# Optimization experiments

Measured on AMD Instinct MI355X. Metric: run time of the kernel, lower is better.

Reference implementation:

```python
import jax, jax.numpy as jnp
import numpy as np

B, N = 4, 500
C_DIM = 256            # content_dim == feat_channels
G = 4                  # n_groups
P_IN, P_OUT = 32, 128
EFF = C_DIM // G       # 64 = eff_in_dim = eff_out_dim
TOTAL = EFF * EFF + P_IN * P_OUT   # 8192 params per group per query
STRIDES = (8, 16, 32, 64)
LVL_SHAPES = ((100, 160), (50, 80), (25, 40), (13, 20))
TAU = 2.0
LVL_MAP = 3.0          # log2(STRIDES[0]): z -> fpn level index
EPS = 1e-5


def setup_inputs() -> dict:
    key = jax.random.key(0)
    ks = jax.random.split(key, 16)
    feats = [jax.random.normal(ks[i], (B, C_DIM, h, w), jnp.float32)
             for i, (h, w) in enumerate(LVL_SHAPES)]
    query_feat = jax.random.normal(ks[4], (B, N, C_DIM), jnp.float32)
    xy = jax.random.uniform(ks[5], (B, N, 2), jnp.float32, 50.0, 1000.0)
    z = jax.random.uniform(ks[6], (B, N, 1), jnp.float32, 3.0, 6.0)
    r = jax.random.uniform(ks[7], (B, N, 1), jnp.float32, -1.0, 1.0)
    query_xyzr = jnp.concatenate([xy, z, r], -1)
    w_off = jax.random.normal(ks[8], (C_DIM, P_IN * G * 3), jnp.float32) * 0.01
    b_off = jax.random.normal(ks[9], (P_IN * G * 3,), jnp.float32) * 0.1
    w_pg = jax.random.normal(ks[10], (C_DIM, G * TOTAL), jnp.float32) * 0.02
    b_pg = jax.random.normal(ks[11], (G * TOTAL,), jnp.float32) * 0.02
    w_out = jax.random.normal(ks[12], (G * P_OUT * EFF, C_DIM), jnp.float32) * 0.005
    b_out = jnp.zeros((C_DIM,), jnp.float32)
    ln_g = jnp.ones((C_DIM,), jnp.float32)
    ln_b = jnp.zeros((C_DIM,), jnp.float32)
    return dict(feat0=feats[0], feat1=feats[1], feat2=feats[2], feat3=feats[3],
                query_feat=query_feat, query_xyzr=query_xyzr,
                w_off=w_off, b_off=b_off, w_pg=w_pg, b_pg=b_pg,
                w_out=w_out, b_out=b_out, ln_g=ln_g, ln_b=ln_b)


def _ln2d(x):
    # F.layer_norm over last TWO dims, no affine
    mu = x.mean((-2, -1), keepdims=True)
    var = jnp.mean((x - mu) ** 2, (-2, -1), keepdims=True)
    return (x - mu) * jax.lax.rsqrt(var + EPS)


def _bilinear(feat, px, py):
    # torch grid_sample(bilinear, zeros padding, align_corners=False)
    # feat: [BG, H, W, Cg]; px, py: [BG, Q] pixel coords
    BGn, H, W, Cg = feat.shape
    fflat = feat.reshape(BGn, H * W, Cg)
    bidx = jnp.arange(BGn)[:, None]
    x0 = jnp.floor(px)
    y0 = jnp.floor(py)
    wx, wy = px - x0, py - y0
    x0i, y0i = x0.astype(jnp.int32), y0.astype(jnp.int32)

    def corner(xi, yi, w):
        valid = (xi >= 0) & (xi < W) & (yi >= 0) & (yi < H)
        idx = jnp.clip(yi, 0, H - 1) * W + jnp.clip(xi, 0, W - 1)
        return fflat[bidx, idx] * (w * valid)[..., None]

    return (corner(x0i, y0i, (1 - wx) * (1 - wy)) + corner(x0i + 1, y0i, wx * (1 - wy))
            + corner(x0i, y0i + 1, (1 - wx) * wy) + corner(x0i + 1, y0i + 1, wx * wy))


def _forward(feat0, feat1, feat2, feat3, query_feat, query_xyzr,
             w_off, b_off, w_pg, b_pg, w_out, b_out, ln_g, ln_b):
    feats = (feat0, feat1, feat2, feat3)
    # --- make_sample_points ---
    off = (query_feat @ w_off + b_off).reshape(B, N, G * P_IN, 3)
    cc = query_xyzr[..., :2]
    z = query_xyzr[..., 2:3]
    r = query_xyzr[..., 3:4]
    roi_wh = (2.0 ** z) * jnp.concatenate([2.0 ** (-0.5 * r), 2.0 ** (0.5 * r)], -1)  # [B,N,2]
    sample_xy = cc[:, :, None, :] + off[..., :2] * roi_wh[:, :, None, :]   # [B,N,G*P,2]
    sample_lvl = z[:, :, None, 0:1] + off[..., 2:3]                        # [B,N,G*P,1]

    # --- sampling_3d: softmax level weights ---
    lvl = sample_lvl[..., 0] - LVL_MAP                                     # [B,N,G*P]
    grid = jnp.arange(len(STRIDES), dtype=lvl.dtype)
    lw = jax.nn.softmax(-((lvl[..., None] - grid) ** 2) / TAU, axis=-1)    # [B,N,G*P,L]

    # regroup to per-group layout [B*G, N*P, ...]
    sx = sample_xy.reshape(B, N, G, P_IN, 2).transpose(0, 2, 1, 3, 4).reshape(B * G, N * P_IN, 2)
    lw_g = lw.reshape(B, N, G, P_IN, -1).transpose(0, 2, 1, 3, 4).reshape(B * G, N * P_IN, -1)

    sampled = jnp.zeros((B * G, N * P_IN, EFF), jnp.float32)
    for li, (feat, stride) in enumerate(zip(feats, STRIDES)):
        H, W = feat.shape[2], feat.shape[3]
        fg = feat.reshape(B * G, EFF, H, W).transpose(0, 2, 3, 1)  # [BG,H,W,EFF]
        nx = sx[..., 0] / (W * stride) * 2.0 - 1.0
        ny = sx[..., 1] / (H * stride) * 2.0 - 1.0
        px = (nx + 1.0) * 0.5 * W - 0.5
        py = (ny + 1.0) * 0.5 * H - 0.5
        sampled = sampled + _bilinear(fg, px, py) * lw_g[..., li][..., None]
    # [B,N,G,P,EFF]
    x = sampled.reshape(B, G, N, P_IN, EFF).transpose(0, 2, 1, 3, 4)

    # --- AdaptiveMixing ---
    params = (query_feat @ w_pg + b_pg).reshape(B * N, G, TOTAL)
    M = params[..., :EFF * EFF].reshape(B * N, G, EFF, EFF)
    S = params[..., EFF * EFF:].reshape(B * N, G, P_OUT, P_IN)
    out = x.reshape(B * N, G, P_IN, EFF)
    out = jax.nn.relu(_ln2d(jnp.einsum('bgpc,bgcd->bgpd', out, M)))  # channel mix
    out = jax.nn.relu(_ln2d(jnp.einsum('bgop,bgpd->bgod', S, out)))  # spatial mix
    out = out.reshape(B, N, G * P_OUT * EFF) @ w_out + b_out
    q = query_feat + out

    # --- final LayerNorm(content_dim) with affine ---
    mu = q.mean(-1, keepdims=True)
    var = jnp.mean((q - mu) ** 2, -1, keepdims=True)
    return (q - mu) * jax.lax.rsqrt(var + EPS) * ln_g + ln_b


def reference(feat0, feat1, feat2, feat3, query_feat, query_xyzr,
              w_off, b_off, w_pg, b_pg, w_out, b_out, ln_g, ln_b):
    return _forward(feat0, feat1, feat2, feat3, query_feat, query_xyzr,
                    w_off, b_off, w_pg, b_pg, w_out, b_out, ln_g, ln_b)
```

## Files before the change

### kernel.cpp

```cpp
#include <hip/hip_runtime.h>
#include <hip/hip_bf16.h>
#include <cstdint>
#include <cstddef>

#define DI __device__ __forceinline__

#define NN 500
#define NQ 2000
#define GTOT 32768
#define LN_EPS 1e-5f

typedef __attribute__((ext_vector_type(8))) short short8v;
typedef __attribute__((ext_vector_type(4))) float f32x4;
typedef const __attribute__((address_space(1))) void* gp1_t;
typedef __attribute__((address_space(3))) void* lp3_t;

DI unsigned short f2bf(float f){
  unsigned u = __float_as_uint(f);
  return (unsigned short)((u + 0x7fffu + ((u>>16)&1u)) >> 16);
}
DI float bf2f(unsigned short s){ return __uint_as_float(((unsigned)s)<<16); }

DI void bred256(float& s, float& s2, float* red, int tid){
  #pragma unroll
  for(int off=32; off; off>>=1){
    s  += __shfl_xor(s,  off, 64);
    s2 += __shfl_xor(s2, off, 64);
  }
  int w = tid>>6;
  if((tid&63)==0){ red[w*2]=s; red[w*2+1]=s2; }
  __syncthreads();
  s  = red[0]+red[2]+red[4]+red[6];
  s2 = red[1]+red[3]+red[5]+red[7];
  __syncthreads();
}

__global__ __launch_bounds__(256) void k_transpose(const float* __restrict__ src,
    unsigned short* __restrict__ dst, int H, int W){
  __shared__ float tile[64][161];
  int bg = blockIdx.x / H, h = blockIdx.x % H;
  int b = bg >> 2, g = bg & 3;
  const float* s = src + (((size_t)(b*256 + g*64))*H + h)*(size_t)W;
  for(int idx=threadIdx.x; idx<64*W; idx+=256){
    int c = idx / W, w = idx - c*W;
    tile[c][w] = s[(size_t)c*H*W + w];
  }
  __syncthreads();
  unsigned short* d = dst + ((size_t)bg*H + h)*(size_t)W*64;
  for(int idx=threadIdx.x; idx<64*W; idx+=256){
    int w = idx>>6, c = idx&63;
    d[idx] = f2bf(tile[c][w]);
  }
}

__global__ __launch_bounds__(384) void k_off(const float* __restrict__ qf,
    const float* __restrict__ xyzr, const float* __restrict__ w_off,
    const float* __restrict__ b_off, float2* __restrict__ xyb, float4* __restrict__ lwb){
  __shared__ float qs[8][256];
  __shared__ float os[8][384];
  int q0 = blockIdx.x*8, tid = threadIdx.x;
  for(int idx=tid; idx<2048; idx+=384){
    int qq = idx>>8, k = idx&255;
    qs[qq][k] = qf[(size_t)(q0+qq)*256 + k];
  }
  __syncthreads();
  {
    int j = tid;
    float acc[8];
    #pragma unroll
    for(int i=0;i<8;i++) acc[i]=0.f;
    for(int k=0;k<256;k++){
      float w = w_off[(size_t)k*384 + j];
      #pragma unroll
      for(int qq=0;qq<8;qq++) acc[qq] += qs[qq][k]*w;
    }
    float bb = b_off[j];
    #pragma unroll
    for(int qq=0;qq<8;qq++) os[qq][j] = acc[qq] + bb;
  }
  __syncthreads();
  for(int idx=tid; idx<1024; idx+=384){
    int qq = idx>>7, gp = idx&127;
    int q = q0+qq;
    float4 xr = *(const float4*)&xyzr[(size_t)q*4];
    float rw = exp2f(xr.z - 0.5f*xr.w);
    float rh = exp2f(xr.z + 0.5f*xr.w);
    float sx = xr.x + os[qq][gp*3+0]*rw;
    float sy = xr.y + os[qq][gp*3+1]*rh;
    float lvl = xr.z + os[qq][gp*3+2] - 3.0f;
    float d0=lvl, d1=lvl-1.f, d2=lvl-2.f, d3=lvl-3.f;
    float e0=-0.5f*d0*d0, e1=-0.5f*d1*d1, e2=-0.5f*d2*d2, e3=-0.5f*d3*d3;
    float m = fmaxf(fmaxf(e0,e1),fmaxf(e2,e3));
    float x0=expf(e0-m), x1=expf(e1-m), x2=expf(e2-m), x3=expf(e3-m);
    float inv = 1.f/(x0+x1+x2+x3);
    xyb[(size_t)q*128+gp] = make_float2(sx,sy);
    lwb[(size_t)q*128+gp] = make_float4(x0*inv, x1*inv, x2*inv, x3*inv);
  }
}

__global__ __launch_bounds__(256) void k_cvtqf(const float* __restrict__ qf,
    unsigned short* __restrict__ qfb){
  int idx = blockIdx.x*256 + threadIdx.x;
  size_t base = (size_t)idx*8;
  int row = idx >> 5;
  ushort4 lo, hi;
  if(row < NQ){
    float4 a = *(const float4*)(qf + base);
    float4 b = *(const float4*)(qf + base + 4);
    lo.x=f2bf(a.x); lo.y=f2bf(a.y); lo.z=f2bf(a.z); lo.w=f2bf(a.w);
    hi.x=f2bf(b.x); hi.y=f2bf(b.y); hi.z=f2bf(b.z); hi.w=f2bf(b.w);
  } else {
    lo.x=lo.y=lo.z=lo.w=0; hi.x=hi.y=hi.z=hi.w=0;
  }
  *(ushort4*)(qfb + base) = lo;
  *(ushort4*)(qfb + base + 4) = hi;
}

__global__ __launch_bounds__(256) void k_trcvt(const float* __restrict__ src,
    unsigned short* __restrict__ dst, int R, int C){
  __shared__ float tile[64][65];
  int ctiles = C >> 6;
  int rt = blockIdx.x / ctiles, ct = blockIdx.x % ctiles;
  int r0 = rt<<6, c0 = ct<<6;
  int tid = threadIdx.x;
  int lr = tid>>6, lc = tid&63;
  #pragma unroll
  for(int i=0;i<16;i++)
    tile[lr + i*4][lc] = src[(size_t)(r0+lr+i*4)*C + c0+lc];
  __syncthreads();
  #pragma unroll
  for(int i=0;i<16;i++)
    dst[(size_t)(c0+lr+i*4)*R + r0+lc] = f2bf(tile[lc][lr+i*4]);
}

DI f32x4 mfma16(short8v a, short8v b, f32x4 c){
  return __builtin_amdgcn_mfma_f32_16x16x32_bf16(a, b, c, 0, 0, 0);
}

DI int swz32(int c, int r){ return c ^ (r&3) ^ ((r>>2)&3); }

DI void stageG32(const unsigned short* __restrict__ g, size_t row0, size_t ldk,
                 size_t k0, unsigned short* lds, int tid){
  int wv = tid>>6;
  #pragma unroll
  for(int i=0;i<2;i++){
    int e = i*256 + tid;
    int r = e>>2, c = e&3;
    int cs = swz32(c, r);
    const unsigned short* gp = g + (row0 + (size_t)r)*ldk + k0 + (size_t)cs*8;
    unsigned short* lp = lds + (size_t)(i*256 + wv*64)*8;
    __builtin_amdgcn_global_load_lds((gp1_t)(const void*)gp, (lp3_t)(void*)lp, 16, 0, 0);
  }
}

DI short8v frag32(const unsigned short* lds, int row, int q4){
  return *(const short8v*)(lds + (size_t)row*32 + (size_t)swz32(q4, row)*8);
}

DI void mma32(const unsigned short* lsA, const unsigned short* lsB,
              int wm, int wn, int lane, f32x4 acc[4][4]){
  int r15 = lane&15, q4 = lane>>4;
  short8v a[4], b[4];
  #pragma unroll
  for(int i=0;i<4;i++){
    a[i] = frag32(lsA, wm*64 + i*16 + r15, q4);
    b[i] = frag32(lsB, wn*64 + i*16 + r15, q4);
  }
  #pragma unroll
  for(int mi=0;mi<4;mi++)
    #pragma unroll
    for(int ni=0;ni<4;ni++)
      acc[mi][ni] = mfma16(a[mi], b[ni], acc[mi][ni]);
}

DI int xcd_remap(int bid, int nwg){
  return ((bid & 7) * (nwg >> 3)) + (bid >> 3);
}

__global__ __launch_bounds__(256, 4) void k_pgemm_mfma(const unsigned short* __restrict__ qfb,
    const unsigned short* __restrict__ wpgT, const float* __restrict__ b_pg,
    unsigned short* __restrict__ par, int qbase, int qlim, int mtiles){
  __shared__ unsigned short pool[16384];
  int bid = xcd_remap(blockIdx.x, gridDim.x);
  int mt = bid % mtiles, nt = bid / mtiles;
  size_t m0 = (size_t)mt*128, n0 = (size_t)nt*128;
  int tid = threadIdx.x, lane = tid&63, wv = tid>>6;
  int wm = wv>>1, wn = wv&1;
  int r15 = lane&15, q4 = lane>>4;
  f32x4 acc[4][4] = {};
  stageG32(qfb,  qbase+m0, 256, 0, pool, tid);
  stageG32(wpgT, n0,       256, 0, pool + 8192, tid);
  __syncthreads();
  #pragma unroll
  for(int t=0; t<8; t++){
    int co = (t&1)*4096;
    if(t<7){
      int no = ((t&1)^1)*4096;
      stageG32(qfb,  qbase+m0, 256, (size_t)(t+1)*32, pool + no, tid);
      stageG32(wpgT, n0,       256, (size_t)(t+1)*32, pool + 8192 + no, tid);
    }
    mma32(pool + co, pool + 8192 + co, wm, wn, lane, acc);
    __syncthreads();
  }
  unsigned short* es = pool;
  #pragma unroll
  for(int h=0; h<2; ++h){
    if(h) __syncthreads();
    if(wn == h){
      #pragma unroll
      for(int ni=0; ni<4; ni++){
        float bias = b_pg[(int)n0 + wn*64 + ni*16 + r15];
        #pragma unroll
        for(int mi=0; mi<4; mi++)
          #pragma unroll
          for(int j=0; j<4; j++){
            int row = wm*64 + mi*16 + q4*4 + j;
            es[row*72 + ni*16 + r15] = f2bf(acc[mi][ni][j] + bias);
          }
      }
    }
    __syncthreads();
    #pragma unroll
    for(int i=0;i<4;i++){
      int e = i*256 + tid;
      int row = e>>3, c8 = (e&7)*8;
      int rl = (int)m0 + row;
      if(qbase + rl < qlim){
        uint4 v = *(const uint4*)(es + row*72 + c8);
        *(uint4*)&par[(size_t)rl*GTOT + n0 + h*64 + c8] = v;
      }
    }
  }
}

__global__ __launch_bounds__(256, 4) void k_fgemm_mfma(const unsigned short* __restrict__ Ag,
    const unsigned short* __restrict__ woutT, float* __restrict__ part,
    int qbase, int qlim, int mtiles, int kspl){
  __shared__ unsigned short pool[16384];
  int bid = xcd_remap(blockIdx.x, gridDim.x);
  int nt = bid & 1;
  int r2 = bid >> 1;
  int mt = r2 % mtiles, ks = r2 / mtiles;
  size_t m0 = (size_t)mt*128, n0 = (size_t)nt*128;
  int tid = threadIdx.x, lane = tid&63, wv = tid>>6;
  int wm = wv>>1, wn = wv&1;
  f32x4 acc[4][4] = {};
  int klen = GTOT / kspl;
  size_t kbase = (size_t)ks*klen;
  int NT = klen >> 5;
  stageG32(Ag,    m0, GTOT, kbase, pool, tid);
  stageG32(woutT, n0, GTOT, kbase, pool + 8192, tid);
  __syncthreads();
  for(int t=0; t<NT; t++){
    int co = (t&1)*4096;
    if(t+1<NT){
      int no = ((t&1)^1)*4096;
      stageG32(Ag,    m0, GTOT, kbase + (size_t)(t+1)*32, pool + no, tid);
      stageG32(woutT, n0, GTOT, kbase + (size_t)(t+1)*32, pool + 8192 + no, tid);
    }
    mma32(pool + co, pool + 8192 + co, wm, wn, lane, acc);
    __syncthreads();
  }
  float* pp = part + (size_t)ks*NQ*256;
  int r15 = lane&15, q4 = lane>>4;
  #pragma unroll
  for(int mi=0; mi<4; mi++){
    #pragma unroll
    for(int j=0; j<4; j++){
      int rl = (int)m0 + wm*64 + mi*16 + q4*4 + j;
      int q = qbase + rl;
      if(q < qlim){
        #pragma unroll
        for(int ni=0; ni<4; ni++){
          int col = (int)n0 + wn*64 + ni*16 + r15;
          pp[(size_t)q*256 + col] = acc[mi][ni][j];
        }
      }
    }
  }
}

__global__ __launch_bounds__(256) void k_mix(const unsigned short* __restrict__ featT,
    const float2* __restrict__ xyb, const float4* __restrict__ lwb,
    const unsigned short* __restrict__ par, unsigned short* __restrict__ out2,
    int qbase){
  __shared__ __align__(16) char poolA[23040];
  __shared__ __align__(16) unsigned short Ss[128*40];
  __shared__ float red[8];
  float* offW = (float*)poolA;
  unsigned short* xs  = (unsigned short*)(poolA + 4096);
  unsigned short* Ms  = (unsigned short*)(poolA + 4096 + 4608);
  unsigned short* o1t = (unsigned short*)(poolA + 4096 + 4608 + 9216);
  unsigned short* o2s = (unsigned short*)poolA;

  int lq = blockIdx.x >> 2, g = blockIdx.x & 3;
  int q = qbase + lq;
  int b = q / NN;
  int bg = b*4 + g;
  int tid = threadIdx.x;
  int lane = tid & 63, wv = tid >> 6;

  const int HH[4] = {100,50,25,13};
  const int WW[4] = {160,80,40,20};
  const float IS[4] = {0.125f, 0.0625f, 0.03125f, 0.015625f};
  const int LO[4] = {0, 16384000, 20480000, 21504000};

  const unsigned short* pb = par + (size_t)lq*GTOT + (size_t)g*8192;
  uint4 mraw0 = *(const uint4*)(pb + tid*8);
  uint4 mraw1 = *(const uint4*)(pb + 2048 + tid*8);
  uint4 sraw0 = *(const uint4*)(pb + 4096 + tid*8);
  uint4 sraw1 = *(const uint4*)(pb + 6144 + tid*8);

  if(tid < 128){
    int p = tid >> 2, l = tid & 3;
    int pi = q*128 + g*32 + p;
    float2 xy = xyb[pi];
    float lw4 = ((const float*)lwb)[(size_t)pi*4 + l];
    int H = HH[l], W = WW[l];
    float px = xy.x*IS[l] - 0.5f;
    float py = xy.y*IS[l] - 0.5f;
    float xf = floorf(px), yf = floorf(py);
    float wx = px - xf, wy = py - yf;
    int x0 = (int)xf, y0 = (int)yf;
    int x1 = x0 + 1, y1 = y0 + 1;
    bool vx0 = (x0>=0)&&(x0<W), vx1 = (x1>=0)&&(x1<W);
    bool vy0 = (y0>=0)&&(y0<H), vy1 = (y1>=0)&&(y1<H);
    int x0c = min(max(x0,0),W-1), x1c = min(max(x1,0),W-1);
    int y0c = min(max(y0,0),H-1), y1c = min(max(y1,0),H-1);
    int base = LO[l] + bg*H*W*64;
    float* e = offW + tid*8;
    e[0] = __int_as_float(base + (y0c*W + x0c)*64);
    e[1] = __int_as_float(base + (y0c*W + x1c)*64);
    e[2] = __int_as_float(base + (y1c*W + x0c)*64);
    e[3] = __int_as_float(base + (y1c*W + x1c)*64);
    e[4] = (1.f-wx)*(1.f-wy)*lw4*(float)(vx0&&vy0);
    e[5] = wx*(1.f-wy)*lw4*(float)(vx1&&vy0);
    e[6] = (1.f-wx)*wy*lw4*(float)(vx0&&vy1);
    e[7] = wx*wy*lw4*(float)(vx1&&vy1);
  }

  {
    int idx0 = tid*8;
    int c0 = idx0>>6, d0 = idx0&63;
    *(uint4*)(Ms + c0*72 + d0) = mraw0;
    int idx1 = 2048 + tid*8;
    int c1 = idx1>>6, d1 = idx1&63;
    *(uint4*)(Ms + c1*72 + d1) = mraw1;
    int o0 = idx0>>5, p0 = idx0&31;
    *(uint4*)(Ss + o0*40 + p0) = sraw0;
    int o1_ = idx1>>5, p1 = idx1&31;
    *(uint4*)(Ss + o1_*40 + p1) = sraw1;
  }
  __syncthreads();

  #pragma unroll
  for(int i=0;i<8;i++){
    int p = wv*8 + i;
    const float* e = offW + p*32;
    float acc = 0.f;
    #pragma unroll
    for(int l=0;l<4;l++){
      const float* el = e + l*8;
      int o00 = __float_as_int(el[0]), o01 = __float_as_int(el[1]);
      int o10 = __float_as_int(el[2]), o11 = __float_as_int(el[3]);
      acc += el[4]*bf2f(featT[o00 + lane]);
      acc += el[5]*bf2f(featT[o01 + lane]);
      acc += el[6]*bf2f(featT[o10 + lane]);
      acc += el[7]*bf2f(featT[o11 + lane]);
    }
    xs[p*72 + lane] = f2bf(acc);
  }
  __syncthreads();

  int r = lane & 15, q4 = lane >> 4;

  {
    short8v af00 = *(const short8v*)(xs + r*72 + q4*8);
    short8v af01 = *(const short8v*)(xs + r*72 + 32 + q4*8);
    short8v af10 = *(const short8v*)(xs + (16+r)*72 + q4*8);
    short8v af11 = *(const short8v*)(xs + (16+r)*72 + 32 + q4*8);
    short8v bm0, bm1;
    #pragma unroll
    for(int j=0;j<8;j++){
      bm0[j] = (short)Ms[(8*q4+j)*72 + wv*16 + r];
      bm1[j] = (short)Ms[(32+8*q4+j)*72 + wv*16 + r];
    }
    f32x4 a0 = {}, a1 = {};
    a0 = mfma16(af00, bm0, a0); a0 = mfma16(af01, bm1, a0);
    a1 = mfma16(af10, bm0, a1); a1 = mfma16(af11, bm1, a1);

    float s = 0.f, s2 = 0.f;
    #pragma unroll
    for(int v=0;v<4;v++){ s += a0[v]+a1[v]; s2 += a0[v]*a0[v] + a1[v]*a1[v]; }
    bred256(s, s2, red, tid);
    float mean = s*(1.f/2048.f);
    float var = s2*(1.f/2048.f) - mean*mean;
    float rs = rsqrtf(var + LN_EPS);
    #pragma unroll
    for(int v=0;v<4;v++){
      float f0 = (a0[v]-mean)*rs; f0 = f0>0.f ? f0 : 0.f;
      float f1 = (a1[v]-mean)*rs; f1 = f1>0.f ? f1 : 0.f;
      o1t[(wv*16+r)*40 + 4*q4 + v] = f2bf(f0);
      o1t[(wv*16+r)*40 + 16 + 4*q4 + v] = f2bf(f1);
    }
  }
  __syncthreads();

  {
    short8v sa0 = *(const short8v*)(Ss + ((wv*2+0)*16 + r)*40 + q4*8);
    short8v sa1 = *(const short8v*)(Ss + ((wv*2+1)*16 + r)*40 + q4*8);
    short8v ov0 = *(const short8v*)(o1t + (r)*40 + q4*8);
    short8v ov1 = *(const short8v*)(o1t + (16+r)*40 + q4*8);
    short8v ov2 = *(const short8v*)(o1t + (32+r)*40 + q4*8);
    short8v ov3 = *(const short8v*)(o1t + (48+r)*40 + q4*8);
    f32x4 c2[2][4] = {};
    c2[0][0] = mfma16(sa0, ov0, c2[0][0]); c2[0][1] = mfma16(sa0, ov1, c2[0][1]);
    c2[0][2] = mfma16(sa0, ov2, c2[0][2]); c2[0][3] = mfma16(sa0, ov3, c2[0][3]);
    c2[1][0] = mfma16(sa1, ov0, c2[1][0]); c2[1][1] = mfma16(sa1, ov1, c2[1][1]);
    c2[1][2] = mfma16(sa1, ov2, c2[1][2]); c2[1][3] = mfma16(sa1, ov3, c2[1][3]);

    float s = 0.f, s2 = 0.f;
    #pragma unroll
    for(int m=0;m<2;m++)
      #pragma unroll
      for(int ni=0;ni<4;ni++)
        #pragma unroll
        for(int v=0;v<4;v++){ float x = c2[m][ni][v]; s += x; s2 += x*x; }
    bred256(s, s2, red, tid);
    float mean = s*(1.f/8192.f);
    float var = s2*(1.f/8192.f) - mean*mean;
    float rs = rsqrtf(var + LN_EPS);
    #pragma unroll
    for(int m=0;m<2;m++)
      #pragma unroll
      for(int ni=0;ni<4;ni++)
        #pragma unroll
        for(int v=0;v<4;v++){
          float x = (c2[m][ni][v]-mean)*rs; x = x>0.f ? x : 0.f;
          int o = (wv*2+m)*16 + 4*q4 + v;
          int d = ni*16 + r;
          o2s[o*72 + d] = f2bf(x);
        }
  }
  __syncthreads();

  unsigned short* og = out2 + (size_t)lq*GTOT + (size_t)g*8192;
  #pragma unroll
  for(int i=0;i<32;i++){
    int row = wv*32 + i;
    og[row*64 + lane] = o2s[row*72 + lane];
  }
}

__global__ __launch_bounds__(256) void k_ln(const float* __restrict__ part,
    const float* __restrict__ qf, const float* __restrict__ b_out,
    const float* __restrict__ ln_g, const float* __restrict__ ln_b,
    float* __restrict__ out, int kspl){
  __shared__ float red[8];
  int q = blockIdx.x, j = threadIdx.x;
  float s = qf[(size_t)q*256 + j] + b_out[j];
  for(int ks=0; ks<kspl; ks++) s += part[((size_t)ks*NQ + q)*256 + j];
  float a = s, a2 = s*s;
  bred256(a, a2, red, j);
  float mean = a*(1.f/256.f);
  float var = a2*(1.f/256.f) - mean*mean;
  float rs = rsqrtf(var + LN_EPS);
  out[(size_t)q*256 + j] = (s-mean)*rs*ln_g[j] + ln_b[j];
}

extern "C" void kernel_launch(void* const* d_in, const int* in_sizes, int n_in,
                              void* d_out, int out_size, void* d_ws, size_t ws_size,
                              hipStream_t stream) {
  const float* feat0 = (const float*)d_in[0];
  const float* feat1 = (const float*)d_in[1];
  const float* feat2 = (const float*)d_in[2];
  const float* feat3 = (const float*)d_in[3];
  const float* qf    = (const float*)d_in[4];
  const float* xyzr  = (const float*)d_in[5];
  const float* w_off = (const float*)d_in[6];
  const float* b_off = (const float*)d_in[7];
  const float* w_pg  = (const float*)d_in[8];
  const float* b_pg  = (const float*)d_in[9];
  const float* w_out = (const float*)d_in[10];
  const float* b_out = (const float*)d_in[11];
  const float* ln_g  = (const float*)d_in[12];
  const float* ln_b  = (const float*)d_in[13];

  const int cand_ksp[5] = {32,16,16,16,16};
  const int cand_nc [5] = { 1, 1, 2, 4, 8};
  int KSP=0, NC=0, qcount=0, qpad=0;
  size_t oFEAT=0,oXY=0,oLW=0,oPART=0,oQFB=0,oWPGT=0,oWOUT=0,oPAR=0;
  for(int ci=0; ci<5; ci++){
    size_t o = 0;
    auto al = [&](size_t bytes){ size_t r = o; o = (o + bytes + 255) & ~255ull; return r; };
    size_t tFEAT = al(43540480ull);
    size_t tXY   = al((size_t)NQ*128*8);
    size_t tLW   = al((size_t)NQ*128*16);
    size_t tPART = al((size_t)cand_ksp[ci]*NQ*256*4);
    size_t tQFB  = al((size_t)2048*256*2);
    size_t tWPGT = al((size_t)GTOT*256*2);
    size_t tWOUT = al((size_t)256*GTOT*2);
    int qc = NQ / cand_nc[ci];
    int qp = (qc + 127) & ~127;
    size_t tPAR = al((size_t)qp*GTOT*2);
    if(o <= ws_size){
      KSP=cand_ksp[ci]; NC=cand_nc[ci]; qcount=qc; qpad=qp;
      oFEAT=tFEAT; oXY=tXY; oLW=tLW; oPART=tPART; oQFB=tQFB; oWPGT=tWPGT; oWOUT=tWOUT; oPAR=tPAR;
      break;
    }
  }
  if(NC == 0) return;

  char* ws = (char*)d_ws;
  unsigned short* featT = (unsigned short*)(ws + oFEAT);
  float2* xyb = (float2*)(ws + oXY);
  float4* lwb = (float4*)(ws + oLW);
  float* part = (float*)(ws + oPART);
  unsigned short* qfb  = (unsigned short*)(ws + oQFB);
  unsigned short* wpgT = (unsigned short*)(ws + oWPGT);
  unsigned short* woutT= (unsigned short*)(ws + oWOUT);
  unsigned short* par  = (unsigned short*)(ws + oPAR);
  unsigned short* o2   = par;

  k_transpose<<<16*100, 256, 0, stream>>>(feat0, featT + 0ull,        100, 160);
  k_transpose<<<16*50,  256, 0, stream>>>(feat1, featT + 16384000ull,  50,  80);
  k_transpose<<<16*25,  256, 0, stream>>>(feat2, featT + 20480000ull,  25,  40);
  k_transpose<<<16*13,  256, 0, stream>>>(feat3, featT + 21504000ull,  13,  20);
  k_off<<<250, 384, 0, stream>>>(qf, xyzr, w_off, b_off, xyb, lwb);
  k_cvtqf<<<256, 256, 0, stream>>>(qf, qfb);
  k_trcvt<<<2048, 256, 0, stream>>>(w_pg,  wpgT, 256, GTOT);
  k_trcvt<<<2048, 256, 0, stream>>>(w_out, woutT, GTOT, 256);

  int mtiles = qpad / 128;
  for (int c = 0; c < NC; ++c) {
    int qbase = c * qcount;
    int qlim  = qbase + qcount;
    k_pgemm_mfma<<<mtiles*256, 256, 0, stream>>>(qfb, wpgT, b_pg, par, qbase, qlim, mtiles);
    k_mix<<<qcount*4, 256, 0, stream>>>(featT, xyb, lwb, par, o2, qbase);
    k_fgemm_mfma<<<mtiles*2*KSP, 256, 0, stream>>>(o2, woutT, part, qbase, qlim, mtiles, KSP);
  }
  k_ln<<<NQ, 256, 0, stream>>>(part, qf, b_out, ln_g, ln_b, (float*)d_out, KSP);
}
```

Baseline: 333.3 us.

## Merge prep kernels into one launch and gather bf16 pairs in mix sampling

Eight preprocessing launches (feature transposes, offset projection, query conversion, weight transposes) are merged into one kernel that dispatches on block index, cutting launch overhead and letting the independent stages run concurrently. The bilinear gather in the mix kernel now has each lane load two adjacent bf16 channels as one 32-bit word for two sample points per iteration, which halves the number of gather instructions. The offset stage now runs with 256 threads instead of 384, so some threads take two columns, and the merged kernel's shared-memory footprint is sized for its largest branch, which may lower occupancy for the smaller branches.

```diff
diff --git a/kernel.cpp b/kernel.cpp
--- a/kernel.cpp
+++ b/kernel.cpp
@@ -35,102 +35,114 @@
   __syncthreads();
 }
 
-__global__ __launch_bounds__(256) void k_transpose(const float* __restrict__ src,
-    unsigned short* __restrict__ dst, int H, int W){
-  __shared__ float tile[64][161];
-  int bg = blockIdx.x / H, h = blockIdx.x % H;
-  int b = bg >> 2, g = bg & 3;
-  const float* s = src + (((size_t)(b*256 + g*64))*H + h)*(size_t)W;
-  for(int idx=threadIdx.x; idx<64*W; idx+=256){
-    int c = idx / W, w = idx - c*W;
-    tile[c][w] = s[(size_t)c*H*W + w];
-  }
-  __syncthreads();
-  unsigned short* d = dst + ((size_t)bg*H + h)*(size_t)W*64;
-  for(int idx=threadIdx.x; idx<64*W; idx+=256){
-    int w = idx>>6, c = idx&63;
-    d[idx] = f2bf(tile[c][w]);
-  }
-}
-
-__global__ __launch_bounds__(384) void k_off(const float* __restrict__ qf,
-    const float* __restrict__ xyzr, const float* __restrict__ w_off,
-    const float* __restrict__ b_off, float2* __restrict__ xyb, float4* __restrict__ lwb){
-  __shared__ float qs[8][256];
-  __shared__ float os[8][384];
-  int q0 = blockIdx.x*8, tid = threadIdx.x;
-  for(int idx=tid; idx<2048; idx+=384){
-    int qq = idx>>8, k = idx&255;
-    qs[qq][k] = qf[(size_t)(q0+qq)*256 + k];
-  }
-  __syncthreads();
-  {
-    int j = tid;
-    float acc[8];
-    #pragma unroll
-    for(int i=0;i<8;i++) acc[i]=0.f;
-    for(int k=0;k<256;k++){
-      float w = w_off[(size_t)k*384 + j];
-      #pragma unroll
-      for(int qq=0;qq<8;qq++) acc[qq] += qs[qq][k]*w;
-    }
-    float bb = b_off[j];
-    #pragma unroll
-    for(int qq=0;qq<8;qq++) os[qq][j] = acc[qq] + bb;
-  }
-  __syncthreads();
-  for(int idx=tid; idx<1024; idx+=384){
-    int qq = idx>>7, gp = idx&127;
-    int q = q0+qq;
-    float4 xr = *(const float4*)&xyzr[(size_t)q*4];
-    float rw = exp2f(xr.z - 0.5f*xr.w);
-    float rh = exp2f(xr.z + 0.5f*xr.w);
-    float sx = xr.x + os[qq][gp*3+0]*rw;
-    float sy = xr.y + os[qq][gp*3+1]*rh;
-    float lvl = xr.z + os[qq][gp*3+2] - 3.0f;
-    float d0=lvl, d1=lvl-1.f, d2=lvl-2.f, d3=lvl-3.f;
-    float e0=-0.5f*d0*d0, e1=-0.5f*d1*d1, e2=-0.5f*d2*d2, e3=-0.5f*d3*d3;
-    float m = fmaxf(fmaxf(e0,e1),fmaxf(e2,e3));
-    float x0=expf(e0-m), x1=expf(e1-m), x2=expf(e2-m), x3=expf(e3-m);
-    float inv = 1.f/(x0+x1+x2+x3);
-    xyb[(size_t)q*128+gp] = make_float2(sx,sy);
-    lwb[(size_t)q*128+gp] = make_float4(x0*inv, x1*inv, x2*inv, x3*inv);
-  }
-}
-
-__global__ __launch_bounds__(256) void k_cvtqf(const float* __restrict__ qf,
-    unsigned short* __restrict__ qfb){
-  int idx = blockIdx.x*256 + threadIdx.x;
-  size_t base = (size_t)idx*8;
-  int row = idx >> 5;
-  ushort4 lo, hi;
-  if(row < NQ){
-    float4 a = *(const float4*)(qf + base);
-    float4 b = *(const float4*)(qf + base + 4);
-    lo.x=f2bf(a.x); lo.y=f2bf(a.y); lo.z=f2bf(a.z); lo.w=f2bf(a.w);
-    hi.x=f2bf(b.x); hi.y=f2bf(b.y); hi.z=f2bf(b.z); hi.w=f2bf(b.w);
+__global__ __launch_bounds__(256) void k_prep(
+    const float* __restrict__ f0, const float* __restrict__ f1,
+    const float* __restrict__ f2, const float* __restrict__ f3,
+    const float* __restrict__ qf, const float* __restrict__ xyzr,
+    const float* __restrict__ w_off, const float* __restrict__ b_off,
+    const float* __restrict__ w_pg, const float* __restrict__ w_out,
+    unsigned short* __restrict__ featT, float2* __restrict__ xyb,
+    float4* __restrict__ lwb, unsigned short* __restrict__ qfb,
+    unsigned short* __restrict__ wpgT, unsigned short* __restrict__ woutT){
+  __shared__ __align__(16) char P[41216];
+  int bid = blockIdx.x, tid = threadIdx.x;
+
+  if(bid < 3008){
+    const float* src; unsigned short* dst; int H, W, lb;
+    if(bid < 1600){ src=f0; dst=featT;            H=100; W=160; lb=bid; }
+    else if(bid < 2400){ src=f1; dst=featT+16384000; H=50; W=80; lb=bid-1600; }
+    else if(bid < 2800){ src=f2; dst=featT+20480000; H=25; W=40; lb=bid-2400; }
+    else { src=f3; dst=featT+21504000; H=13; W=20; lb=bid-2800; }
+    float (*tile)[161] = (float(*)[161])P;
+    int bg = lb / H, h = lb % H;
+    int b = bg >> 2, g = bg & 3;
+    const float* s = src + (((size_t)(b*256 + g*64))*H + h)*(size_t)W;
+    for(int idx=tid; idx<64*W; idx+=256){
+      int c = idx / W, w = idx - c*W;
+      tile[c][w] = s[(size_t)c*H*W + w];
+    }
+    __syncthreads();
+    unsigned short* d = dst + ((size_t)bg*H + h)*(size_t)W*64;
+    for(int idx=tid; idx<64*W; idx+=256){
+      int w = idx>>6, c = idx&63;
+      d[idx] = f2bf(tile[c][w]);
+    }
+  } else if(bid < 3264){
+    int idx = (bid-3008)*256 + tid;
+    size_t base = (size_t)idx*8;
+    int row = idx >> 5;
+    ushort4 lo, hi;
+    if(row < NQ){
+      float4 a = *(const float4*)(qf + base);
+      float4 b = *(const float4*)(qf + base + 4);
+      lo.x=f2bf(a.x); lo.y=f2bf(a.y); lo.z=f2bf(a.z); lo.w=f2bf(a.w);
+      hi.x=f2bf(b.x); hi.y=f2bf(b.y); hi.z=f2bf(b.z); hi.w=f2bf(b.w);
+    } else {
+      lo.x=lo.y=lo.z=lo.w=0; hi.x=hi.y=hi.z=hi.w=0;
+    }
+    *(ushort4*)(qfb + base) = lo;
+    *(ushort4*)(qfb + base + 4) = hi;
+  } else if(bid < 7360){
+    const float* src; unsigned short* dst; int R, C, lb;
+    if(bid < 5312){ src=w_pg;  dst=wpgT;  R=256;  C=GTOT; lb=bid-3264; }
+    else          { src=w_out; dst=woutT; R=GTOT; C=256;  lb=bid-5312; }
+    float (*tile)[65] = (float(*)[65])P;
+    int ctiles = C >> 6;
+    int rt = lb / ctiles, ct = lb % ctiles;
+    int r0 = rt<<6, c0 = ct<<6;
+    int lr = tid>>6, lc = tid&63;
+    #pragma unroll
+    for(int i=0;i<16;i++)
+      tile[lr + i*4][lc] = src[(size_t)(r0+lr+i*4)*C + c0+lc];
+    __syncthreads();
+    #pragma unroll
+    for(int i=0;i<16;i++)
+      dst[(size_t)(c0+lr+i*4)*R + r0+lc] = f2bf(tile[lc][lr+i*4]);
   } else {
-    lo.x=lo.y=lo.z=lo.w=0; hi.x=hi.y=hi.z=hi.w=0;
-  }
-  *(ushort4*)(qfb + base) = lo;
-  *(ushort4*)(qfb + base + 4) = hi;
-}
-
-__global__ __launch_bounds__(256) void k_trcvt(const float* __restrict__ src,
-    unsigned short* __restrict__ dst, int R, int C){
-  __shared__ float tile[64][65];
-  int ctiles = C >> 6;
-  int rt = blockIdx.x / ctiles, ct = blockIdx.x % ctiles;
-  int r0 = rt<<6, c0 = ct<<6;
-  int tid = threadIdx.x;
-  int lr = tid>>6, lc = tid&63;
-  #pragma unroll
-  for(int i=0;i<16;i++)
-    tile[lr + i*4][lc] = src[(size_t)(r0+lr+i*4)*C + c0+lc];
-  __syncthreads();
-  #pragma unroll
-  for(int i=0;i<16;i++)
-    dst[(size_t)(c0+lr+i*4)*R + r0+lc] = f2bf(tile[lc][lr+i*4]);
+    float (*qs)[256] = (float(*)[256])P;
+    float (*os)[384] = (float(*)[384])(P + 8192);
+    int q0 = (bid-7360)*8;
+    for(int idx=tid; idx<2048; idx+=256){
+      int qq = idx>>8, k = idx&255;
+      qs[qq][k] = qf[(size_t)(q0+qq)*256 + k];
+    }
+    __syncthreads();
+    #pragma unroll
+    for(int jj=0; jj<2; jj++){
+      int j = tid + jj*256;
+      if(j < 384){
+        float acc[8];
+        #pragma unroll
+        for(int i=0;i<8;i++) acc[i]=0.f;
+        for(int k=0;k<256;k++){
+          float w = w_off[(size_t)k*384 + j];
+          #pragma unroll
+          for(int qq=0;qq<8;qq++) acc[qq] += qs[qq][k]*w;
+        }
+        float bb = b_off[j];
+        #pragma unroll
+        for(int qq=0;qq<8;qq++) os[qq][j] = acc[qq] + bb;
+      }
+    }
+    __syncthreads();
+    for(int idx=tid; idx<1024; idx+=256){
+      int qq = idx>>7, gp = idx&127;
+      int q = q0+qq;
+      float4 xr = *(const float4*)&xyzr[(size_t)q*4];
+      float rw = exp2f(xr.z - 0.5f*xr.w);
+      float rh = exp2f(xr.z + 0.5f*xr.w);
+      float sx = xr.x + os[qq][gp*3+0]*rw;
+      float sy = xr.y + os[qq][gp*3+1]*rh;
+      float lvl = xr.z + os[qq][gp*3+2] - 3.0f;
+      float d0=lvl, d1=lvl-1.f, d2=lvl-2.f, d3=lvl-3.f;
+      float e0=-0.5f*d0*d0, e1=-0.5f*d1*d1, e2=-0.5f*d2*d2, e3=-0.5f*d3*d3;
+      float m = fmaxf(fmaxf(e0,e1),fmaxf(e2,e3));
+      float x0=expf(e0-m), x1=expf(e1-m), x2=expf(e2-m), x3=expf(e3-m);
+      float inv = 1.f/(x0+x1+x2+x3);
+      xyb[(size_t)q*128+gp] = make_float2(sx,sy);
+      lwb[(size_t)q*128+gp] = make_float4(x0*inv, x1*inv, x2*inv, x3*inv);
+    }
+  }
 }
 
 DI f32x4 mfma16(short8v a, short8v b, f32x4 c){
@@ -353,22 +365,30 @@
   }
   __syncthreads();
 
-  #pragma unroll
-  for(int i=0;i<8;i++){
-    int p = wv*8 + i;
-    const float* e = offW + p*32;
-    float acc = 0.f;
-    #pragma unroll
-    for(int l=0;l<4;l++){
-      const float* el = e + l*8;
-      int o00 = __float_as_int(el[0]), o01 = __float_as_int(el[1]);
-      int o10 = __float_as_int(el[2]), o11 = __float_as_int(el[3]);
-      acc += el[4]*bf2f(featT[o00 + lane]);
-      acc += el[5]*bf2f(featT[o01 + lane]);
-      acc += el[6]*bf2f(featT[o10 + lane]);
-      acc += el[7]*bf2f(featT[o11 + lane]);
-    }
-    xs[p*72 + lane] = f2bf(acc);
+  {
+    int half = lane >> 5, cp = lane & 31;
+    const unsigned short* fb_ = featT + cp*2;
+    #pragma unroll
+    for(int i=0;i<4;i++){
+      int p = wv*8 + i*2 + half;
+      const float* e = offW + p*32;
+      float aLo = 0.f, aHi = 0.f;
+      #pragma unroll
+      for(int l=0;l<4;l++){
+        float4 ea = *(const float4*)(e + l*8);
+        float4 eb = *(const float4*)(e + l*8 + 4);
+        unsigned u00 = *(const unsigned*)(fb_ + __float_as_int(ea.x));
+        unsigned u01 = *(const unsigned*)(fb_ + __float_as_int(ea.y));
+        unsigned u10 = *(const unsigned*)(fb_ + __float_as_int(ea.z));
+        unsigned u11 = *(const unsigned*)(fb_ + __float_as_int(ea.w));
+        aLo += eb.x*__uint_as_float(u00<<16); aHi += eb.x*__uint_as_float(u00&0xffff0000u);
+        aLo += eb.y*__uint_as_float(u01<<16); aHi += eb.y*__uint_as_float(u01&0xffff0000u);
+        aLo += eb.z*__uint_as_float(u10<<16); aHi += eb.z*__uint_as_float(u10&0xffff0000u);
+        aLo += eb.w*__uint_as_float(u11<<16); aHi += eb.w*__uint_as_float(u11&0xffff0000u);
+      }
+      unsigned lo = f2bf(aLo), hi = f2bf(aHi);
+      *(unsigned*)(xs + p*72 + cp*2) = lo | (hi<<16);
+    }
   }
   __syncthreads();
 
@@ -522,14 +542,8 @@
   unsigned short* par  = (unsigned short*)(ws + oPAR);
   unsigned short* o2   = par;
 
-  k_transpose<<<16*100, 256, 0, stream>>>(feat0, featT + 0ull,        100, 160);
-  k_transpose<<<16*50,  256, 0, stream>>>(feat1, featT + 16384000ull,  50,  80);
-  k_transpose<<<16*25,  256, 0, stream>>>(feat2, featT + 20480000ull,  25,  40);
-  k_transpose<<<16*13,  256, 0, stream>>>(feat3, featT + 21504000ull,  13,  20);
-  k_off<<<250, 384, 0, stream>>>(qf, xyzr, w_off, b_off, xyb, lwb);
-  k_cvtqf<<<256, 256, 0, stream>>>(qf, qfb);
-  k_trcvt<<<2048, 256, 0, stream>>>(w_pg,  wpgT, 256, GTOT);
-  k_trcvt<<<2048, 256, 0, stream>>>(w_out, woutT, GTOT, 256);
+  k_prep<<<7610, 256, 0, stream>>>(feat0, feat1, feat2, feat3, qf, xyzr,
+      w_off, b_off, w_pg, w_out, featT, xyb, lwb, qfb, wpgT, woutT);
 
   int mtiles = qpad / 128;
   for (int c = 0; c < NC; ++c) {
```

After: 321.0 us. -3.7%, faster.

## Vectorize transpose/convert kernels and gather two channels per lane in mix

Applied to the files above, without the earlier changes.

Replaces the LDS-tiled feature and weight transposes with register-level 4x4 transposes that use float4 loads and ushort4 stores. This removes the shared-memory round trip and the scalar global stores. In the mixing kernel's bilinear gather, each lane now loads two adjacent bf16 channels as one 32-bit word and handles two sample points per wave-half, halving the number of gather loads. The new transposes produce wider but less contiguous store patterns, and the gather relies on 4-byte alignment of the offsets.

```diff
diff --git a/kernel.cpp b/kernel.cpp
--- a/kernel.cpp
+++ b/kernel.cpp
@@ -21,6 +21,10 @@
 }
 DI float bf2f(unsigned short s){ return __uint_as_float(((unsigned)s)<<16); }
 
+DI ushort4 cvt4(float4 a){
+  ushort4 r; r.x=f2bf(a.x); r.y=f2bf(a.y); r.z=f2bf(a.z); r.w=f2bf(a.w); return r;
+}
+
 DI void bred256(float& s, float& s2, float* red, int tid){
   #pragma unroll
   for(int off=32; off; off>>=1){
@@ -33,24 +37,6 @@
   s  = red[0]+red[2]+red[4]+red[6];
   s2 = red[1]+red[3]+red[5]+red[7];
   __syncthreads();
-}
-
-__global__ __launch_bounds__(256) void k_transpose(const float* __restrict__ src,
-    unsigned short* __restrict__ dst, int H, int W){
-  __shared__ float tile[64][161];
-  int bg = blockIdx.x / H, h = blockIdx.x % H;
-  int b = bg >> 2, g = bg & 3;
-  const float* s = src + (((size_t)(b*256 + g*64))*H + h)*(size_t)W;
-  for(int idx=threadIdx.x; idx<64*W; idx+=256){
-    int c = idx / W, w = idx - c*W;
-    tile[c][w] = s[(size_t)c*H*W + w];
-  }
-  __syncthreads();
-  unsigned short* d = dst + ((size_t)bg*H + h)*(size_t)W*64;
-  for(int idx=threadIdx.x; idx<64*W; idx+=256){
-    int w = idx>>6, c = idx&63;
-    d[idx] = f2bf(tile[c][w]);
-  }
 }
 
 __global__ __launch_bounds__(384) void k_off(const float* __restrict__ qf,
@@ -107,8 +93,7 @@
   if(row < NQ){
     float4 a = *(const float4*)(qf + base);
     float4 b = *(const float4*)(qf + base + 4);
-    lo.x=f2bf(a.x); lo.y=f2bf(a.y); lo.z=f2bf(a.z); lo.w=f2bf(a.w);
-    hi.x=f2bf(b.x); hi.y=f2bf(b.y); hi.z=f2bf(b.z); hi.w=f2bf(b.w);
+    lo = cvt4(a); hi = cvt4(b);
   } else {
     lo.x=lo.y=lo.z=lo.w=0; hi.x=hi.y=hi.z=hi.w=0;
   }
@@ -118,19 +103,48 @@
 
 __global__ __launch_bounds__(256) void k_trcvt(const float* __restrict__ src,
     unsigned short* __restrict__ dst, int R, int C){
-  __shared__ float tile[64][65];
   int ctiles = C >> 6;
   int rt = blockIdx.x / ctiles, ct = blockIdx.x % ctiles;
   int r0 = rt<<6, c0 = ct<<6;
-  int tid = threadIdx.x;
-  int lr = tid>>6, lc = tid&63;
-  #pragma unroll
-  for(int i=0;i<16;i++)
-    tile[lr + i*4][lc] = src[(size_t)(r0+lr+i*4)*C + c0+lc];
-  __syncthreads();
-  #pragma unroll
-  for(int i=0;i<16;i++)
-    dst[(size_t)(c0+lr+i*4)*R + r0+lc] = f2bf(tile[lc][lr+i*4]);
+  int t = threadIdx.x;
+  int tr = t >> 4, tc = t & 15;
+  int r = r0 + tr*4, c = c0 + tc*4;
+  float4 v0 = *(const float4*)(src + (size_t)(r+0)*C + c);
+  float4 v1 = *(const float4*)(src + (size_t)(r+1)*C + c);
+  float4 v2 = *(const float4*)(src + (size_t)(r+2)*C + c);
+  float4 v3 = *(const float4*)(src + (size_t)(r+3)*C + c);
+  ushort4 o0 = make_ushort4(f2bf(v0.x), f2bf(v1.x), f2bf(v2.x), f2bf(v3.x));
+  ushort4 o1 = make_ushort4(f2bf(v0.y), f2bf(v1.y), f2bf(v2.y), f2bf(v3.y));
+  ushort4 o2 = make_ushort4(f2bf(v0.z), f2bf(v1.z), f2bf(v2.z), f2bf(v3.z));
+  ushort4 o3 = make_ushort4(f2bf(v0.w), f2bf(v1.w), f2bf(v2.w), f2bf(v3.w));
+  *(ushort4*)(dst + (size_t)(c+0)*R + r) = o0;
+  *(ushort4*)(dst + (size_t)(c+1)*R + r) = o1;
+  *(ushort4*)(dst + (size_t)(c+2)*R + r) = o2;
+  *(ushort4*)(dst + (size_t)(c+3)*R + r) = o3;
+}
+
+__global__ __launch_bounds__(256) void k_featT(const float* __restrict__ src,
+    unsigned short* __restrict__ dst, int HW, int nb){
+  int bg = blockIdx.x / nb, hb = blockIdx.x % nb;
+  int b = bg >> 2, g = bg & 3;
+  const float* s = src + ((size_t)(b*256 + g*64))*HW;
+  unsigned short* d = dst + (size_t)bg*HW*64;
+  int t = threadIdx.x;
+  int tc = t >> 4, th = t & 15;
+  int c = tc*4, hw = hb*64 + th*4;
+  if(hw >= HW) return;
+  float4 v0 = *(const float4*)(s + (size_t)(c+0)*HW + hw);
+  float4 v1 = *(const float4*)(s + (size_t)(c+1)*HW + hw);
+  float4 v2 = *(const float4*)(s + (size_t)(c+2)*HW + hw);
+  float4 v3 = *(const float4*)(s + (size_t)(c+3)*HW + hw);
+  ushort4 o0 = make_ushort4(f2bf(v0.x), f2bf(v1.x), f2bf(v2.x), f2bf(v3.x));
+  ushort4 o1 = make_ushort4(f2bf(v0.y), f2bf(v1.y), f2bf(v2.y), f2bf(v3.y));
+  ushort4 o2 = make_ushort4(f2bf(v0.z), f2bf(v1.z), f2bf(v2.z), f2bf(v3.z));
+  ushort4 o3 = make_ushort4(f2bf(v0.w), f2bf(v1.w), f2bf(v2.w), f2bf(v3.w));
+  *(ushort4*)(d + (size_t)(hw+0)*64 + c) = o0;
+  *(ushort4*)(d + (size_t)(hw+1)*64 + c) = o1;
+  *(ushort4*)(d + (size_t)(hw+2)*64 + c) = o2;
+  *(ushort4*)(d + (size_t)(hw+3)*64 + c) = o3;
 }
 
 DI f32x4 mfma16(short8v a, short8v b, f32x4 c){
@@ -353,22 +367,30 @@
   }
   __syncthreads();
 
-  #pragma unroll
-  for(int i=0;i<8;i++){
-    int p = wv*8 + i;
-    const float* e = offW + p*32;
-    float acc = 0.f;
-    #pragma unroll
-    for(int l=0;l<4;l++){
-      const float* el = e + l*8;
-      int o00 = __float_as_int(el[0]), o01 = __float_as_int(el[1]);
-      int o10 = __float_as_int(el[2]), o11 = __float_as_int(el[3]);
-      acc += el[4]*bf2f(featT[o00 + lane]);
-      acc += el[5]*bf2f(featT[o01 + lane]);
-      acc += el[6]*bf2f(featT[o10 + lane]);
-      acc += el[7]*bf2f(featT[o11 + lane]);
-    }
-    xs[p*72 + lane] = f2bf(acc);
+  {
+    int half = lane >> 5, cp = lane & 31;
+    const unsigned short* fb_ = featT + cp*2;
+    #pragma unroll
+    for(int i=0;i<4;i++){
+      int p = wv*8 + i*2 + half;
+      const float* e = offW + p*32;
+      float aLo = 0.f, aHi = 0.f;
+      #pragma unroll
+      for(int l=0;l<4;l++){
+        float4 ea = *(const float4*)(e + l*8);
+        float4 eb = *(const float4*)(e + l*8 + 4);
+        unsigned u00 = *(const unsigned*)(fb_ + __float_as_int(ea.x));
+        unsigned u01 = *(const unsigned*)(fb_ + __float_as_int(ea.y));
+        unsigned u10 = *(const unsigned*)(fb_ + __float_as_int(ea.z));
+        unsigned u11 = *(const unsigned*)(fb_ + __float_as_int(ea.w));
+        aLo += eb.x*__uint_as_float(u00<<16); aHi += eb.x*__uint_as_float(u00&0xffff0000u);
+        aLo += eb.y*__uint_as_float(u01<<16); aHi += eb.y*__uint_as_float(u01&0xffff0000u);
+        aLo += eb.z*__uint_as_float(u10<<16); aHi += eb.z*__uint_as_float(u10&0xffff0000u);
+        aLo += eb.w*__uint_as_float(u11<<16); aHi += eb.w*__uint_as_float(u11&0xffff0000u);
+      }
+      unsigned lo = f2bf(aLo), hi = f2bf(aHi);
+      *(unsigned*)(xs + p*72 + cp*2) = lo | (hi<<16);
+    }
   }
   __syncthreads();
 
@@ -522,14 +544,14 @@
   unsigned short* par  = (unsigned short*)(ws + oPAR);
   unsigned short* o2   = par;
 
-  k_transpose<<<16*100, 256, 0, stream>>>(feat0, featT + 0ull,        100, 160);
-  k_transpose<<<16*50,  256, 0, stream>>>(feat1, featT + 16384000ull,  50,  80);
-  k_transpose<<<16*25,  256, 0, stream>>>(feat2, featT + 20480000ull,  25,  40);
-  k_transpose<<<16*13,  256, 0, stream>>>(feat3, featT + 21504000ull,  13,  20);
   k_off<<<250, 384, 0, stream>>>(qf, xyzr, w_off, b_off, xyb, lwb);
   k_cvtqf<<<256, 256, 0, stream>>>(qf, qfb);
   k_trcvt<<<2048, 256, 0, stream>>>(w_pg,  wpgT, 256, GTOT);
   k_trcvt<<<2048, 256, 0, stream>>>(w_out, woutT, GTOT, 256);
+  k_featT<<<16*250, 256, 0, stream>>>(feat0, featT + 0,        16000, 250);
+  k_featT<<<16*63,  256, 0, stream>>>(feat1, featT + 16384000, 4000,  63);
+  k_featT<<<16*16,  256, 0, stream>>>(feat2, featT + 20480000, 1000,  16);
+  k_featT<<<16*5,   256, 0, stream>>>(feat3, featT + 21504000, 260,   5);
 
   int mtiles = qpad / 128;
   for (int c = 0; c < NC; ++c) {
```

Result: no change. 329.7 us (-1.1%).
